# Kernel optimization log

Measured on AMD Instinct MI355X. Metric: run time of the kernel, lower is better.

Reference implementation:

```python
import jax, jax.numpy as jnp
import numpy as np

NUM_FEATURES = 128   # conv spatial length
WINDOW = 128         # conv channels / lstm seq len
KC = 16              # kernels per group
KS = 3               # conv kernel size
FC1 = 32             # number of independent LSTMs
H = 32               # lstm hidden size
NL = 2               # lstm layers
PAD = 1
POOL_LEN = (NUM_FEATURES + 2 * PAD) // 2  # maxpool(k=2,s=2,p=1) output length
B = 128


def setup_inputs():
    key = jax.random.key(0)
    ks = jax.random.split(key, 13)
    x = jax.random.normal(ks[0], (B, WINDOW, NUM_FEATURES), jnp.float32)
    conv_w = jax.random.normal(ks[1], (WINDOW * KC, 1, KS), jnp.float32) * 0.3
    conv_b = jax.random.normal(ks[2], (WINDOW * KC,), jnp.float32) * 0.1
    fc1_in = KC * POOL_LEN
    fc1_w = jax.random.normal(ks[3], (FC1, fc1_in), jnp.float32) * 0.02
    fc1_b = jax.random.normal(ks[4], (FC1,), jnp.float32) * 0.02
    w_ih0 = jax.random.normal(ks[5], (FC1, 4 * H), jnp.float32) * 0.1          # layer0, input size 1
    w_ih1 = jax.random.normal(ks[6], (NL - 1, FC1, 4 * H, H), jnp.float32) * 0.1
    w_hh = jax.random.normal(ks[7], (NL, FC1, 4 * H, H), jnp.float32) * 0.1
    b_lstm = jax.random.normal(ks[8], (NL, FC1, 4 * H), jnp.float32) * 0.1     # bias_ih + bias_hh combined
    mu_w = jax.random.normal(ks[9], (1, FC1 * H), jnp.float32) * 0.05
    mu_b = jax.random.normal(ks[10], (1,), jnp.float32) * 0.05
    lv_w = jax.random.normal(ks[11], (1, FC1 * H), jnp.float32) * 0.05
    lv_b = jax.random.normal(ks[12], (1,), jnp.float32) * 0.05
    return {"x": x, "conv_w": conv_w, "conv_b": conv_b, "fc1_w": fc1_w, "fc1_b": fc1_b,
            "w_ih0": w_ih0, "w_ih1": w_ih1, "w_hh": w_hh, "b_lstm": b_lstm,
            "mu_w": mu_w, "mu_b": mu_b, "lv_w": lv_w, "lv_b": lv_b}


def _lstm_cell(gates, c_prev):
    # torch gate order: i, f, g, o
    i, f, g, o = jnp.split(gates, 4, axis=-1)
    c_new = jax.nn.sigmoid(f) * c_prev + jax.nn.sigmoid(i) * jnp.tanh(g)
    h_new = jax.nn.sigmoid(o) * jnp.tanh(c_new)
    return h_new, c_new


def reference(x, conv_w, conv_b, fc1_w, fc1_b, w_ih0, w_ih1, w_hh, b_lstm, mu_w, mu_b, lv_w, lv_b):
    bsz = x.shape[0]
    # grouped conv1d: groups = WINDOW, each group maps 1 -> KC channels
    y = jax.lax.conv_general_dilated(x, conv_w, window_strides=(1,), padding=[(PAD, PAD)],
                                     feature_group_count=WINDOW,
                                     dimension_numbers=('NCH', 'OIH', 'NCH'))
    y = jax.nn.relu(y + conv_b[None, :, None])
    neg = jnp.finfo(y.dtype).min
    y = jnp.pad(y, ((0, 0), (0, 0), (PAD, PAD)), constant_values=neg)
    y = y.reshape(bsz, WINDOW * KC, POOL_LEN, 2).max(axis=-1)
    # regroup to [B, WINDOW, KC*POOL_LEN] (channel layout = group-major, matches torch view)
    y = y.reshape(bsz, WINDOW, KC * POOL_LEN)
    z = jnp.einsum('bwi,oi->bwo', y, fc1_w) + fc1_b   # [B, WINDOW, FC1]

    # FC1 independent NL-layer LSTMs batched over the feature axis; time axis = WINDOW
    h0 = jnp.zeros((NL, bsz, FC1, H), z.dtype)
    c0 = jnp.zeros_like(h0)

    def step(carry, x_t):  # x_t: [B, FC1]
        h, c = carry
        hs, cs = [], []
        gates = jnp.einsum('bf,fg->bfg', x_t, w_ih0) + jnp.einsum('bfh,fgh->bfg', h[0], w_hh[0]) + b_lstm[0]
        h_l, c_l = _lstm_cell(gates, c[0])
        hs.append(h_l); cs.append(c_l)
        for l in range(1, NL):
            gates = (jnp.einsum('bfh,fgh->bfg', h_l, w_ih1[l - 1])
                     + jnp.einsum('bfh,fgh->bfg', h[l], w_hh[l]) + b_lstm[l])
            h_l, c_l = _lstm_cell(gates, c[l])
            hs.append(h_l); cs.append(c_l)
        return (jnp.stack(hs), jnp.stack(cs)), None

    (h_fin, _), _ = jax.lax.scan(step, (h0, c0), jnp.transpose(z, (1, 0, 2)))
    combined = h_fin[-1].reshape(bsz, FC1 * H)  # top layer, last step; feature-major like torch.cat
    mu = combined @ mu_w.T + mu_b
    log_var = combined @ lv_w.T + lv_b
    sigma = jnp.exp(0.5 * log_var)
    return (mu - 1.96 * sigma, mu, mu + 1.96 * sigma, log_var)
```

## Files before the change

### kernel.cpp

```cpp
#include <hip/hip_runtime.h>
#include <hip/hip_bf16.h>
#include <math.h>

#define BATCH 128
#define WIN   128
#define NF    128
#define KC    16
#define POOL  65
#define NFC1  32
#define HS    32
#define LW    40
#define KP    1056
#define PSTR  1064

typedef float f32x4 __attribute__((ext_vector_type(4)));
typedef short bf16x8 __attribute__((ext_vector_type(8)));

#define LOG2E   1.442695041f
#define LOG2E2  2.885390082f

__device__ __forceinline__ float cellf(float& c, float gi, float gf, float gg, float go) {
    float ei = __builtin_amdgcn_exp2f(gi);
    float ef = __builtin_amdgcn_exp2f(gf);
    float eg = __builtin_amdgcn_exp2f(gg);
    float eo = __builtin_amdgcn_exp2f(go);
    float pf = 1.f + ef;
    float pi = 1.f + ei;
    float pg = eg + 1.f;
    float R3 = __builtin_amdgcn_rcpf(pf * pi * pg);
    float sf = pi * pg * R3;
    c = fmaf(sf, c, (eg - 1.f) * pf * R3);
    float ec = __builtin_amdgcn_exp2f(__builtin_amdgcn_fmed3f(c, -30.f, 30.f) * LOG2E2);
    return (ec - 1.f) * __builtin_amdgcn_rcpf((1.f + eo) * (ec + 1.f));
}
__device__ __forceinline__ unsigned short f2bf(float x) {
    __hip_bfloat16 h = __float2bfloat16(x);
    unsigned short u; __builtin_memcpy(&u, &h, 2); return u;
}
__device__ __forceinline__ float bf2f(unsigned short u) {
    unsigned int v = ((unsigned int)u) << 16;
    float f; __builtin_memcpy(&f, &v, 4); return f;
}
__device__ __forceinline__ bf16x8 load_row8_scaled(const float* row, float sc) {
    float4 lo = ((const float4*)row)[0];
    float4 hi = ((const float4*)row)[1];
    union { bf16x8 v; unsigned short u[8]; } t;
    t.u[0] = f2bf(lo.x * sc); t.u[1] = f2bf(lo.y * sc); t.u[2] = f2bf(lo.z * sc); t.u[3] = f2bf(lo.w * sc);
    t.u[4] = f2bf(hi.x * sc); t.u[5] = f2bf(hi.y * sc); t.u[6] = f2bf(hi.z * sc); t.u[7] = f2bf(hi.w * sc);
    return t.v;
}

__global__ __launch_bounds__(256) void k0_wconv(
    const float* __restrict__ fc1_w, unsigned short* __restrict__ w_bf)
{
    const int o = blockIdx.x;
    for (int i = threadIdx.x; i < KP; i += 256) {
        float v = (i < KC * POOL) ? fc1_w[(size_t)o * (KC * POOL) + i] : 0.f;
        w_bf[(size_t)o * KP + i] = f2bf(v);
    }
}

__global__ __launch_bounds__(256, 4) void k1_conv_fc1(
    const float* __restrict__ x, const float* __restrict__ conv_w, const float* __restrict__ conv_b,
    const unsigned short* __restrict__ w_bf, const float* __restrict__ fc1_b, float* __restrict__ z)
{
    __shared__ __align__(16) unsigned short xp[16][132];
    __shared__ __align__(16) unsigned short poolb[16 * PSTR];
    __shared__ float cw[KC][3];
    __shared__ float cb[KC];
    __shared__ float fb[NFC1];

    const int w = blockIdx.x >> 3;
    const int bbase = (blockIdx.x & 7) * 16;
    const int tid = threadIdx.x;

    if (tid < KC * 3) cw[tid / 3][tid % 3] = conv_w[(w * KC + tid / 3) * 3 + tid % 3];
    if (tid >= 64 && tid < 64 + KC) cb[tid - 64] = conv_b[w * KC + (tid - 64)];
    if (tid >= 96 && tid < 96 + NFC1) fb[tid - 96] = fc1_b[tid - 96];

    for (int i = tid; i < 16 * 32; i += 256) {
        int b = i >> 5, q = i & 31;
        float4 v = ((const float4*)(x + (size_t)(bbase + b) * (WIN * NF) + (size_t)w * NF))[q];
        unsigned short* dst = &xp[b][1 + q * 4];
        dst[0] = f2bf(v.x); dst[1] = f2bf(v.y); dst[2] = f2bf(v.z); dst[3] = f2bf(v.w);
    }
    if (tid < 16) { xp[tid][0] = 0; xp[tid][129] = 0; xp[tid][130] = 0; xp[tid][131] = 0; }
    __syncthreads();

    {
        const int b = tid >> 4;
        const int k = tid & 15;
        const float w0 = cw[k][0], w1 = cw[k][1], w2 = cw[k][2], bb = cb[k];
        float v1 = 0.f;
        float v2 = bf2f(xp[b][0]);
        float v3 = bf2f(xp[b][1]);
        unsigned short* prow = &poolb[b * PSTR + k * POOL];
        #pragma unroll 5
        for (int j = 0; j < POOL; ++j) {
            float v0 = v1; v1 = v2; v2 = v3;
            v3 = bf2f(xp[b][2 * j + 2]);
            float oa = bb + w0 * v0 + w1 * v1 + w2 * v2;
            float ob = bb + w0 * v1 + w1 * v2 + w2 * v3;
            float m = 0.f;
            if (j > 0)        m = fmaxf(m, oa);
            if (j < POOL - 1) m = fmaxf(m, ob);
            prow[j] = f2bf(m);
        }
    }
    for (int i = tid; i < 16 * (KP - KC * POOL); i += 256) {
        int b = i >> 4, c = i & 15;
        poolb[b * PSTR + KC * POOL + c] = 0;
    }
    __syncthreads();

    const int lane = tid & 63;
    const int wid = tid >> 6;
    if (wid < 2) {
        const int col = lane & 15;
        const int kg = lane >> 4;
        const int g = wid * 16 + col;
        f32x4 acc;
        {
            float bias = fb[g];
            acc[0] = bias; acc[1] = bias; acc[2] = bias; acc[3] = bias;
        }
        const unsigned short* wrow = w_bf + (size_t)g * KP;
        #pragma unroll 4
        for (int ks = 0; ks < KP / 32; ++ks) {
            bf16x8 aP = *(const bf16x8*)&poolb[col * PSTR + ks * 32 + kg * 8];
            bf16x8 bW = *(const bf16x8*)&wrow[ks * 32 + kg * 8];
            acc = __builtin_amdgcn_mfma_f32_16x16x32_bf16(aP, bW, acc, 0, 0, 0);
        }
        float4 st; st.x = acc[0]; st.y = acc[1]; st.z = acc[2]; st.w = acc[3];
        *(float4*)&z[(size_t)w * (NFC1 * BATCH) + (size_t)g * BATCH + bbase + kg * 4] = st;
    }
}

__global__ __launch_bounds__(256, 1) void k2_lstm_mfma(
    const float* __restrict__ w_ih0, const float* __restrict__ w_ih1,
    const float* __restrict__ w_hh, const float* __restrict__ b_lstm,
    const float* __restrict__ z, float* __restrict__ h1fin)
{
    __shared__ float zs[WIN][16];
    __shared__ __align__(16) unsigned short h0b0[16 * LW];
    __shared__ __align__(16) unsigned short h0b1[16 * LW];
    __shared__ __align__(16) unsigned short h1b0[16 * LW];
    __shared__ __align__(16) unsigned short h1b1[16 * LW];

    const int f = blockIdx.x >> 3;
    const int bbase = (blockIdx.x & 7) * 16;
    const int tid = threadIdx.x;
    const int wid = tid >> 6, lane = tid & 63;
    const bool isL0 = (wid < 2);
    const int s = wid & 1;
    const int col = lane & 15;
    const int kg = lane >> 4;

    for (int i = tid; i < WIN * 4; i += 256) {
        int t = i >> 2, q = i & 3;
        ((float4*)&zs[t][0])[q] = ((const float4*)&z[(size_t)t * (NFC1 * BATCH) + f * BATCH + bbase])[q];
    }
    for (int i = tid; i < 16 * LW; i += 256) {
        h0b0[i] = 0; h0b1[i] = 0; h1b0[i] = 0; h1b1[i] = 0;
    }

    const float gsc[4] = { -LOG2E, -LOG2E, LOG2E2, -LOG2E };

    const float* WA = isL0 ? (w_hh + (size_t)f * 4096)
                           : (w_ih1 + (size_t)f * 4096);
    const float* WV = w_hh + (size_t)(NFC1 + f) * 4096;
    bf16x8 fA[4], fB[4];
    float bias[4], wi0[4];
    const int loff = isL0 ? 0 : (NFC1 * 128);
    #pragma unroll
    for (int gi = 0; gi < 4; ++gi) {
        int nt = gi * 2 + s;
        int g = nt * 16 + col;
        fA[gi] = load_row8_scaled(WA + g * 32 + kg * 8, gsc[gi]);
        if (!isL0) fB[gi] = load_row8_scaled(WV + g * 32 + kg * 8, gsc[gi]);
        bias[gi] = b_lstm[loff + f * 128 + g] * gsc[gi];
        wi0[gi] = w_ih0[f * 128 + g] * gsc[gi];
    }
    __syncthreads();

    const int hread = col * LW + kg * 8;
    const int hw0 = (kg * 4 + 0) * LW + 16 * s + col;
    float cst[4] = {0.f, 0.f, 0.f, 0.f};
    f32x4 zv = *(const f32x4*)&zs[0][kg * 4];

    auto body = [&](int it, const unsigned short* h0r, unsigned short* h0w,
                            const unsigned short* h1r, unsigned short* h1w) {
        if (isL0) {
            if (it < WIN) {
                bf16x8 hA = *(const bf16x8*)&h0r[hread];
                f32x4 aI, aF, aG, aO;
                #pragma unroll
                for (int j = 0; j < 4; ++j) {
                    aI[j] = fmaf(zv[j], wi0[0], bias[0]);
                    aF[j] = fmaf(zv[j], wi0[1], bias[1]);
                    aG[j] = fmaf(zv[j], wi0[2], bias[2]);
                    aO[j] = fmaf(zv[j], wi0[3], bias[3]);
                }
                aI = __builtin_amdgcn_mfma_f32_16x16x32_bf16(hA, fA[0], aI, 0, 0, 0);
                aF = __builtin_amdgcn_mfma_f32_16x16x32_bf16(hA, fA[1], aF, 0, 0, 0);
                aG = __builtin_amdgcn_mfma_f32_16x16x32_bf16(hA, fA[2], aG, 0, 0, 0);
                aO = __builtin_amdgcn_mfma_f32_16x16x32_bf16(hA, fA[3], aO, 0, 0, 0);
                if (it + 1 < WIN) zv = *(const f32x4*)&zs[it + 1][kg * 4];
                #pragma unroll
                for (int j = 0; j < 4; ++j) {
                    float h = cellf(cst[j], aI[j], aF[j], aG[j], aO[j]);
                    h0w[hw0 + j * LW] = f2bf(h);
                }
            }
        } else {
            if (it >= 1) {
                bf16x8 hA = *(const bf16x8*)&h0r[hread];
                bf16x8 hB = *(const bf16x8*)&h1r[hread];
                f32x4 aI, aF, aG, aO;
                #pragma unroll
                for (int j = 0; j < 4; ++j) { aI[j] = bias[0]; aF[j] = bias[1]; aG[j] = bias[2]; aO[j] = bias[3]; }
                aI = __builtin_amdgcn_mfma_f32_16x16x32_bf16(hA, fA[0], aI, 0, 0, 0);
                aI = __builtin_amdgcn_mfma_f32_16x16x32_bf16(hB, fB[0], aI, 0, 0, 0);
                aF = __builtin_amdgcn_mfma_f32_16x16x32_bf16(hA, fA[1], aF, 0, 0, 0);
                aF = __builtin_amdgcn_mfma_f32_16x16x32_bf16(hB, fB[1], aF, 0, 0, 0);
                aG = __builtin_amdgcn_mfma_f32_16x16x32_bf16(hA, fA[2], aG, 0, 0, 0);
                aG = __builtin_amdgcn_mfma_f32_16x16x32_bf16(hB, fB[2], aG, 0, 0, 0);
                aO = __builtin_amdgcn_mfma_f32_16x16x32_bf16(hA, fA[3], aO, 0, 0, 0);
                aO = __builtin_amdgcn_mfma_f32_16x16x32_bf16(hB, fB[3], aO, 0, 0, 0);
                if (it < WIN) {
                    #pragma unroll
                    for (int j = 0; j < 4; ++j) {
                        float h = cellf(cst[j], aI[j], aF[j], aG[j], aO[j]);
                        h1w[hw0 + j * LW] = f2bf(h);
                    }
                } else {
                    #pragma unroll
                    for (int j = 0; j < 4; ++j) {
                        float h = cellf(cst[j], aI[j], aF[j], aG[j], aO[j]);
                        h1fin[(size_t)(bbase + kg * 4 + j) * (NFC1 * HS) + f * HS + 16 * s + col] = h;
                    }
                }
            }
        }
    };

    body(0, h0b0, h0b1, h1b0, h1b1);
    __syncthreads();
    #pragma unroll 1
    for (int it = 1; it <= WIN; it += 2) {
        body(it,     h0b1, h0b0, h1b1, h1b0);
        __syncthreads();
        body(it + 1, h0b0, h0b1, h1b0, h1b1);
        __syncthreads();
    }
}

__global__ __launch_bounds__(128) void k3_head(
    const float* __restrict__ h1fin, const float* __restrict__ mu_w, const float* __restrict__ mu_b,
    const float* __restrict__ lv_w, const float* __restrict__ lv_b, float* __restrict__ out)
{
    const int b = blockIdx.x, tid = threadIdx.x;
    const float* hrow = h1fin + (size_t)b * (NFC1 * HS);
    float am = 0.f, al = 0.f;
    for (int i = tid; i < NFC1 * HS; i += 128) {
        float h = hrow[i];
        am = fmaf(h, mu_w[i], am);
        al = fmaf(h, lv_w[i], al);
    }
    for (int off = 32; off >= 1; off >>= 1) {
        am += __shfl_down(am, off, 64);
        al += __shfl_down(al, off, 64);
    }
    __shared__ float sm[2], sl[2];
    const int wv = tid >> 6, ln = tid & 63;
    if (ln == 0) { sm[wv] = am; sl[wv] = al; }
    __syncthreads();
    if (tid == 0) {
        float mu = sm[0] + sm[1] + mu_b[0];
        float lv = sl[0] + sl[1] + lv_b[0];
        float sg = expf(0.5f * lv);
        out[b]           = mu - 1.96f * sg;
        out[128 + b]     = mu;
        out[256 + b]     = mu + 1.96f * sg;
        out[384 + b]     = lv;
    }
}

extern "C" void kernel_launch(void* const* d_in, const int* in_sizes, int n_in,
                              void* d_out, int out_size, void* d_ws, size_t ws_size,
                              hipStream_t stream)
{
    const float* x      = (const float*)d_in[0];
    const float* conv_w = (const float*)d_in[1];
    const float* conv_b = (const float*)d_in[2];
    const float* fc1_w  = (const float*)d_in[3];
    const float* fc1_b  = (const float*)d_in[4];
    const float* w_ih0  = (const float*)d_in[5];
    const float* w_ih1  = (const float*)d_in[6];
    const float* w_hh   = (const float*)d_in[7];
    const float* b_lstm = (const float*)d_in[8];
    const float* mu_w   = (const float*)d_in[9];
    const float* mu_b   = (const float*)d_in[10];
    const float* lv_w   = (const float*)d_in[11];
    const float* lv_b   = (const float*)d_in[12];
    float* out = (float*)d_out;

    float* z     = (float*)d_ws;
    float* h1fin = z + (size_t)WIN * NFC1 * BATCH;
    unsigned short* w_bf = (unsigned short*)(h1fin + (size_t)BATCH * NFC1 * HS);

    k0_wconv<<<dim3(NFC1), dim3(256), 0, stream>>>(fc1_w, w_bf);
    k1_conv_fc1<<<dim3(WIN * 8), dim3(256), 0, stream>>>(x, conv_w, conv_b, w_bf, fc1_b, z);
    k2_lstm_mfma<<<dim3(NFC1 * 8), dim3(256), 0, stream>>>(w_ih0, w_ih1, w_hh, b_lstm, z, h1fin);
    k3_head<<<dim3(BATCH), dim3(128), 0, stream>>>(h1fin, mu_w, mu_b, lv_w, lv_b, out);
}
```

Before: 85.30 us.

## Split LSTM batch into 8-row blocks and halve per-lane cell work via shuffles

The LSTM kernel now runs 512 blocks of 8 batch rows instead of 256 blocks of 16. The MFMA tile is padded with zero rows, and lanes exchange accumulator halves with xor-32 shuffles so each lane evaluates only two cell updates instead of four. This targets the serial per-step latency of the transcendental-heavy cell math and doubles the number of blocks for the 256 CUs. The trade-offs are wasted MFMA work on padding rows, extra cross-lane shuffles, and a cellf rewritten to use separate reciprocals. Launch bounds now allow two blocks per CU.

```diff
diff --git a/kernel.cpp b/kernel.cpp
--- a/kernel.cpp
+++ b/kernel.cpp
@@ -24,12 +24,8 @@
     float ef = __builtin_amdgcn_exp2f(gf);
     float eg = __builtin_amdgcn_exp2f(gg);
     float eo = __builtin_amdgcn_exp2f(go);
-    float pf = 1.f + ef;
-    float pi = 1.f + ei;
-    float pg = eg + 1.f;
-    float R3 = __builtin_amdgcn_rcpf(pf * pi * pg);
-    float sf = pi * pg * R3;
-    c = fmaf(sf, c, (eg - 1.f) * pf * R3);
+    float sf = __builtin_amdgcn_rcpf(1.f + ef);
+    c = fmaf(sf, c, (eg - 1.f) * __builtin_amdgcn_rcpf((1.f + ei) * (eg + 1.f)));
     float ec = __builtin_amdgcn_exp2f(__builtin_amdgcn_fmed3f(c, -30.f, 30.f) * LOG2E2);
     return (ec - 1.f) * __builtin_amdgcn_rcpf((1.f + eo) * (ec + 1.f));
 }
@@ -136,7 +132,7 @@
     }
 }
 
-__global__ __launch_bounds__(256, 1) void k2_lstm_mfma(
+__global__ __launch_bounds__(256, 2) void k2_lstm_mfma(
     const float* __restrict__ w_ih0, const float* __restrict__ w_ih1,
     const float* __restrict__ w_hh, const float* __restrict__ b_lstm,
     const float* __restrict__ z, float* __restrict__ h1fin)
@@ -147,18 +143,21 @@
     __shared__ __align__(16) unsigned short h1b0[16 * LW];
     __shared__ __align__(16) unsigned short h1b1[16 * LW];
 
-    const int f = blockIdx.x >> 3;
-    const int bbase = (blockIdx.x & 7) * 16;
+    const int f = blockIdx.x >> 4;
+    const int bbase = (blockIdx.x & 15) * 8;
     const int tid = threadIdx.x;
     const int wid = tid >> 6, lane = tid & 63;
     const bool isL0 = (wid < 2);
     const int s = wid & 1;
     const int col = lane & 15;
     const int kg = lane >> 4;
+    const bool hi = (kg >= 2);
 
     for (int i = tid; i < WIN * 4; i += 256) {
         int t = i >> 2, q = i & 3;
-        ((float4*)&zs[t][0])[q] = ((const float4*)&z[(size_t)t * (NFC1 * BATCH) + f * BATCH + bbase])[q];
+        float4 v = {0.f, 0.f, 0.f, 0.f};
+        if (q < 2) v = ((const float4*)&z[(size_t)t * (NFC1 * BATCH) + f * BATCH + bbase])[q];
+        ((float4*)&zs[t][0])[q] = v;
     }
     for (int i = tid; i < 16 * LW; i += 256) {
         h0b0[i] = 0; h0b1[i] = 0; h1b0[i] = 0; h1b1[i] = 0;
@@ -184,8 +183,11 @@
     __syncthreads();
 
     const int hread = col * LW + kg * 8;
-    const int hw0 = (kg * 4 + 0) * LW + 16 * s + col;
-    float cst[4] = {0.f, 0.f, 0.f, 0.f};
+    const int eidx = 16 * s + col;
+    const int brow0 = hi ? ((kg - 2) * 4 + 2) : (kg * 4);
+    const int wr0 = brow0 * LW + eidx;
+    const int wr1 = wr0 + LW;
+    float cst[2] = {0.f, 0.f};
     f32x4 zv = *(const f32x4*)&zs[0][kg * 4];
 
     auto body = [&](int it, const unsigned short* h0r, unsigned short* h0w,
@@ -206,11 +208,16 @@
                 aG = __builtin_amdgcn_mfma_f32_16x16x32_bf16(hA, fA[2], aG, 0, 0, 0);
                 aO = __builtin_amdgcn_mfma_f32_16x16x32_bf16(hA, fA[3], aO, 0, 0, 0);
                 if (it + 1 < WIN) zv = *(const f32x4*)&zs[it + 1][kg * 4];
-                #pragma unroll
-                for (int j = 0; j < 4; ++j) {
-                    float h = cellf(cst[j], aI[j], aF[j], aG[j], aO[j]);
-                    h0w[hw0 + j * LW] = f2bf(h);
-                }
+                float sI2 = __shfl_xor(aI[2], 32, 64), sI3 = __shfl_xor(aI[3], 32, 64);
+                float sF2 = __shfl_xor(aF[2], 32, 64), sF3 = __shfl_xor(aF[3], 32, 64);
+                float sG2 = __shfl_xor(aG[2], 32, 64), sG3 = __shfl_xor(aG[3], 32, 64);
+                float sO2 = __shfl_xor(aO[2], 32, 64), sO3 = __shfl_xor(aO[3], 32, 64);
+                float h0v = cellf(cst[0], hi ? sI2 : aI[0], hi ? sF2 : aF[0],
+                                          hi ? sG2 : aG[0], hi ? sO2 : aO[0]);
+                float h1v = cellf(cst[1], hi ? sI3 : aI[1], hi ? sF3 : aF[1],
+                                          hi ? sG3 : aG[1], hi ? sO3 : aO[1]);
+                h0w[wr0] = f2bf(h0v);
+                h0w[wr1] = f2bf(h1v);
             }
         } else {
             if (it >= 1) {
@@ -227,18 +234,20 @@
                 aG = __builtin_amdgcn_mfma_f32_16x16x32_bf16(hB, fB[2], aG, 0, 0, 0);
                 aO = __builtin_amdgcn_mfma_f32_16x16x32_bf16(hA, fA[3], aO, 0, 0, 0);
                 aO = __builtin_amdgcn_mfma_f32_16x16x32_bf16(hB, fB[3], aO, 0, 0, 0);
+                float sI2 = __shfl_xor(aI[2], 32, 64), sI3 = __shfl_xor(aI[3], 32, 64);
+                float sF2 = __shfl_xor(aF[2], 32, 64), sF3 = __shfl_xor(aF[3], 32, 64);
+                float sG2 = __shfl_xor(aG[2], 32, 64), sG3 = __shfl_xor(aG[3], 32, 64);
+                float sO2 = __shfl_xor(aO[2], 32, 64), sO3 = __shfl_xor(aO[3], 32, 64);
+                float h0v = cellf(cst[0], hi ? sI2 : aI[0], hi ? sF2 : aF[0],
+                                          hi ? sG2 : aG[0], hi ? sO2 : aO[0]);
+                float h1v = cellf(cst[1], hi ? sI3 : aI[1], hi ? sF3 : aF[1],
+                                          hi ? sG3 : aG[1], hi ? sO3 : aO[1]);
                 if (it < WIN) {
-                    #pragma unroll
-                    for (int j = 0; j < 4; ++j) {
-                        float h = cellf(cst[j], aI[j], aF[j], aG[j], aO[j]);
-                        h1w[hw0 + j * LW] = f2bf(h);
-                    }
+                    h1w[wr0] = f2bf(h0v);
+                    h1w[wr1] = f2bf(h1v);
                 } else {
-                    #pragma unroll
-                    for (int j = 0; j < 4; ++j) {
-                        float h = cellf(cst[j], aI[j], aF[j], aG[j], aO[j]);
-                        h1fin[(size_t)(bbase + kg * 4 + j) * (NFC1 * HS) + f * HS + 16 * s + col] = h;
-                    }
+                    h1fin[(size_t)(bbase + brow0)     * (NFC1 * HS) + f * HS + eidx] = h0v;
+                    h1fin[(size_t)(bbase + brow0 + 1) * (NFC1 * HS) + f * HS + eidx] = h1v;
                 }
             }
         }
@@ -311,6 +320,6 @@
 
     k0_wconv<<<dim3(NFC1), dim3(256), 0, stream>>>(fc1_w, w_bf);
     k1_conv_fc1<<<dim3(WIN * 8), dim3(256), 0, stream>>>(x, conv_w, conv_b, w_bf, fc1_b, z);
-    k2_lstm_mfma<<<dim3(NFC1 * 8), dim3(256), 0, stream>>>(w_ih0, w_ih1, w_hh, b_lstm, z, h1fin);
+    k2_lstm_mfma<<<dim3(NFC1 * 16), dim3(256), 0, stream>>>(w_ih0, w_ih1, w_hh, b_lstm, z, h1fin);
     k3_head<<<dim3(BATCH), dim3(128), 0, stream>>>(h1fin, mu_w, mu_b, lv_w, lv_b, out);
 }
```

Result: slower. 97.51 us (+14.3%).
